# Optimization experiments

Measured on AMD Instinct MI355X. Metric: run time of the kernel, lower is better.

## Reference

```python
import jax, jax.numpy as jnp
import numpy as np

HEADS = 12
C = 384
FS = 56
WS = 7
WN = FS // WS            # windows per side = 8
NW = WN * WN             # total windows = 64
DISP = WS // 2           # cyclic shift displacement = 3
DK = (C / HEADS) ** (-0.5)


def _create_mask(ws, d, zero_dim=False, one_dim=False):
    m = np.zeros((ws * ws, ws * ws), np.float32)
    if zero_dim:
        m[-d * ws:, :-d * ws] = -np.inf
        m[:-d * ws, -d * ws:] = -np.inf
    if one_dim:
        t = np.zeros((ws, ws), np.float32)
        t[-d:, :-d] = -np.inf
        t[:-d, -d:] = -np.inf
        for i in range(0, ws * ws, ws):
            for j in range(0, ws * ws, ws):
                m[i:i + ws, j:j + ws] = t
    return m


def _window_mask():
    # per-window additive mask [NW, WS*WS, WS*WS] matching the torch slicing
    zm = _create_mask(WS, DISP, zero_dim=True)
    om = _create_mask(WS, DISP, one_dim=True)
    wm = np.zeros((NW, WS * WS, WS * WS), np.float32)
    wm[-WN:] += zm                 # last row of windows
    wm[WN - 1::WN] += om           # last column of windows
    return jnp.asarray(wm)


def _rel_indices():
    idx = np.array([[x, y] for x in range(WS) for y in range(WS)], np.int64)
    rel = idx[None, :, :] - idx[:, None, :] + WS - 1   # [WS^2, WS^2, 2]
    return rel


def _dconv(x, w):
    # depthwise 3x3, padding=1
    return jax.lax.conv_general_dilated(
        x, w, (1, 1), ((1, 1), (1, 1)),
        dimension_numbers=('NCHW', 'OIHW', 'NCHW'),
        feature_group_count=w.shape[0])


def _pconv(x, w, b):
    y = jax.lax.conv_general_dilated(
        x, w, (1, 1), 'VALID', dimension_numbers=('NCHW', 'OIHW', 'NCHW'))
    return y + b[None, :, None, None]


def _to_windows(t):
    # [B, C, H, W] -> [B, heads, NW, WS*WS, head_dim]
    B = t.shape[0]
    hd = C // HEADS
    t = t.reshape(B, HEADS, hd, WN, WS, WN, WS)
    t = t.transpose(0, 1, 3, 5, 4, 6, 2)
    return t.reshape(B, HEADS, NW, WS * WS, hd)


def _from_windows(t):
    # [B, heads, NW, WS*WS, head_dim] -> [B, C, H, W]
    B = t.shape[0]
    hd = C // HEADS
    t = t.reshape(B, HEADS, WN, WN, WS, WS, hd)
    t = t.transpose(0, 1, 6, 2, 4, 3, 5)
    return t.reshape(B, C, FS, FS)


def setup_inputs() -> dict:
    key = jax.random.key(0)
    ks = jax.random.split(key, 8)
    s = 0.05
    return {
        'x': jax.random.normal(ks[0], (16, C, FS, FS), jnp.float32),
        'qkv_dw': jax.random.normal(ks[1], (C, 1, 3, 3), jnp.float32) * s,
        'qkv_pw': jax.random.normal(ks[2], (3 * C, C, 1, 1), jnp.float32) * s,
        'qkv_pb': jax.random.normal(ks[3], (3 * C,), jnp.float32) * s,
        'out_dw': jax.random.normal(ks[4], (C, 1, 3, 3), jnp.float32) * s,
        'out_pw': jax.random.normal(ks[5], (C, C, 1, 1), jnp.float32) * s,
        'out_pb': jax.random.normal(ks[6], (C,), jnp.float32) * s,
        'pos_emb': jax.random.normal(ks[7], (2 * WS - 1, 2 * WS - 1), jnp.float32),
    }


def reference(x, qkv_dw, qkv_pw, qkv_pb, out_dw, out_pw, out_pb, pos_emb):
    rel = _rel_indices()
    wmask = _window_mask()

    x = jnp.roll(x, shift=(-DISP, -DISP), axis=(2, 3))       # cyclic shift
    x = _dconv(x, qkv_dw)
    qkv = _pconv(x, qkv_pw, qkv_pb)
    q, k, v = jnp.split(qkv, 3, axis=1)
    q, k, v = _to_windows(q), _to_windows(k), _to_windows(v)

    dots = jnp.einsum('bhwid,bhwjd->bhwij', q, k) * DK
    bias = pos_emb[rel[:, :, 0], rel[:, :, 1]]               # [WS^2, WS^2]
    dots = dots + bias[None, None, None] + wmask[None, None]

    attn = jax.nn.softmax(dots, axis=-1)
    out = jnp.einsum('bhwij,bhwjd->bhwid', attn, v)
    out = _from_windows(out)

    out = jnp.roll(out, shift=(DISP, DISP), axis=(2, 3))     # cyclic back shift
    out = _dconv(out, out_dw)
    out = _pconv(out, out_pw, out_pb)
    return out
```

## Files before the change

kernel.cpp:

```cpp
#include <hip/hip_runtime.h>
#include <hip/hip_bf16.h>
#include <cstddef>
#include <cstdint>

#define BQ    16
#define CC    384
#define C3    1152
#define HH    56
#define HWP   3136
#define NTOT  (BQ * HWP)
#define NHEAD 12
#define HD    32
#define WSZ   7
#define NWIN  64
#define WSQ   49
#define DKS   0.17677669529663687f

typedef __attribute__((ext_vector_type(8))) short bf16x8;
typedef __attribute__((ext_vector_type(4))) float f32x4;

union U128 { uint4 u; bf16x8 v; ushort us[8]; uint ui[4]; };

__device__ __forceinline__ ushort f2b(float f) {
    __hip_bfloat16 h = __float2bfloat16(f);
    return *reinterpret_cast<ushort*>(&h);
}
__device__ __forceinline__ float b2f(ushort u) {
    __hip_bfloat16 h;
    *reinterpret_cast<ushort*>(&h) = u;
    return __bfloat162float(h);
}

__global__ void cvt_bf16(const float* __restrict__ in, ushort* __restrict__ out, int n) {
    const int i = blockIdx.x * 256 + threadIdx.x;
    if (i < n) out[i] = f2b(in[i]);
}

__global__ void prep_mask(const float* __restrict__ pos, float* __restrict__ M) {
    const int idx = blockIdx.x * 256 + threadIdx.x;
    const int v = idx >> 12, rem = idx & 4095;
    const int j = rem >> 6, i = rem & 63;
    float m = -1e30f;
    if (i < WSQ && j < WSQ) {
        const int pir = i / WSZ, pic = i - pir * WSZ;
        const int pjr = j / WSZ, pjc = j - pjr * WSZ;
        const bool msk = ((v & 2) && ((pir >= 4) != (pjr >= 4))) ||
                         ((v & 1) && ((pic >= 4) != (pjc >= 4)));
        m = msk ? -1e30f : pos[(pjr - pir + 6) * 13 + (pjc - pic + 6)];
    }
    M[idx] = m;
}

template <bool BF16IN, int S>
__global__ __launch_bounds__(256) void dconv_px(const void* __restrict__ inv,
                                                const float* __restrict__ dw,
                                                ushort* __restrict__ out) {
    __shared__ ushort pl[6][32][68];
    const int band = blockIdx.x, cg = blockIdx.y, b = blockIdx.z;
    const int i0 = band * 4;
    const int t = threadIdx.x;
    const int ch = t & 31;

    float wreg[9];
    #pragma unroll
    for (int k = 0; k < 9; ++k) wreg[k] = dw[(cg * 32 + ch) * 9 + k];

    if (BF16IN) {
        const ushort* src = (const ushort*)inv;
        const int c8 = t & 3, sc = t >> 2;
        const int cc = sc < 56 ? sc : sc - 56;
        #pragma unroll
        for (int lr = 0; lr < 6; ++lr) {
            const int gi = i0 + lr - 1;
            U128 u; u.u = make_uint4(0, 0, 0, 0);
            if (gi >= 0 && gi < HH) {
                int rr = gi + S; if (rr >= HH) rr -= HH;
                u.u = *(const uint4*)&src[(size_t)(b * HWP + rr * HH + cc) * CC + cg * 32 + c8 * 8];
            }
            #pragma unroll
            for (int k2 = 0; k2 < 8; ++k2) pl[lr][c8 * 8 + k2][sc] = u.us[k2];
        }
    } else {
        const float* src = (const float*)inv;
        const int cq = t & 15, q0 = t >> 4;
        const int scb = cq < 14 ? cq * 4 : cq * 4 - 56;
        #pragma unroll
        for (int k = 0; k < 12; ++k) {
            const int pair = q0 + k * 16;
            const int lc = pair & 31, lr = pair >> 5;
            const int gi = i0 + lr - 1;
            float4 v = make_float4(0.f, 0.f, 0.f, 0.f);
            if (gi >= 0 && gi < HH) {
                int rr = gi + S; if (rr >= HH) rr -= HH;
                v = *(const float4*)&src[((size_t)(b * CC + cg * 32 + lc)) * HWP + rr * HH + scb];
            }
            ushort4 w;
            w.x = f2b(v.x); w.y = f2b(v.y); w.z = f2b(v.z); w.w = f2b(v.w);
            *(ushort4*)&pl[lr][lc][cq * 4] = w;
        }
    }
    __syncthreads();

    const int u = t >> 5;
    #pragma unroll
    for (int iter = 0; iter < 7; ++iter) {
        const int unit = iter * 8 + u;
        const int colb = unit >> 2;
        const int row  = unit & 3;
        const int c0 = colb * 4;
        int sc0 = c0 - 1 + S; if (sc0 >= HH) sc0 -= HH;
        float acc[4] = {0.f, 0.f, 0.f, 0.f};
        #pragma unroll
        for (int di = 0; di < 3; ++di) {
            const ushort* rp = &pl[row + di][ch][0];
            float v[6];
            #pragma unroll
            for (int k = 0; k < 6; ++k) v[k] = b2f(rp[sc0 + k]);
            if (colb == 0)  v[0] = 0.f;
            if (colb == 13) v[5] = 0.f;
            #pragma unroll
            for (int cc2 = 0; cc2 < 4; ++cc2) {
                acc[cc2] += wreg[di * 3 + 0] * v[cc2];
                acc[cc2] += wreg[di * 3 + 1] * v[cc2 + 1];
                acc[cc2] += wreg[di * 3 + 2] * v[cc2 + 2];
            }
        }
        const int orow = i0 + row;
        #pragma unroll
        for (int cc2 = 0; cc2 < 4; ++cc2)
            out[(size_t)(b * HWP + orow * HH + c0 + cc2) * CC + cg * 32 + ch] = f2b(acc[cc2]);
    }
}

template <int OC, bool OUT_BF16>
__global__ __launch_bounds__(256) void pconv_mfma(const ushort* __restrict__ bt,
                                                  const ushort* __restrict__ wa,
                                                  const float* __restrict__ bias,
                                                  void* __restrict__ outv) {
    __shared__ __align__(16) char smem[OUT_BF16 ? 34816 : 32768];

    const int nwg = gridDim.x;
    const int cpx = nwg >> 3;
    const int id  = blockIdx.x;
    const int wg  = (id & 7) * cpx + (id >> 3);
    const int oc0 = (wg % (OC / 128)) * 128;
    const int n0  = (wg / (OC / 128)) * 128;

    const int t   = threadIdx.x;
    const int l   = t & 63;
    const int wm  = (t >> 6) >> 1, wn = (t >> 6) & 1;
    const int i15 = l & 15, g = l >> 4;

    f32x4 acc[4][4] = {};

    const int r0 = t >> 2;
    const int kc = ((t & 3) ^ ((t >> 3) & 3)) * 8;
    const size_t gA0 = (size_t)(oc0 + r0) * CC + kc;
    const size_t gA1 = (size_t)(oc0 + r0 + 64) * CC + kc;
    const size_t gB0 = (size_t)(n0 + r0) * CC + kc;
    const size_t gB1 = (size_t)(n0 + r0 + 64) * CC + kc;
    const int ldsOff = (t & 192) * 16;

#define STAGE(buf, k0) do {                                                              \
    char* la_ = smem + (buf) * 16384 + ldsOff;                                           \
    char* lb_ = la_ + 8192;                                                              \
    __builtin_amdgcn_global_load_lds(                                                    \
        (const __attribute__((address_space(1))) void*)(wa + gA0 + (k0)),                \
        (__attribute__((address_space(3))) void*)la_, 16, 0, 0);                         \
    __builtin_amdgcn_global_load_lds(                                                    \
        (const __attribute__((address_space(1))) void*)(wa + gA1 + (k0)),                \
        (__attribute__((address_space(3))) void*)(la_ + 4096), 16, 0, 0);                \
    __builtin_amdgcn_global_load_lds(                                                    \
        (const __attribute__((address_space(1))) void*)(bt + gB0 + (k0)),                \
        (__attribute__((address_space(3))) void*)lb_, 16, 0, 0);                         \
    __builtin_amdgcn_global_load_lds(                                                    \
        (const __attribute__((address_space(1))) void*)(bt + gB1 + (k0)),                \
        (__attribute__((address_space(3))) void*)(lb_ + 4096), 16, 0, 0);                \
} while (0)

    const int colb = (g ^ ((i15 >> 1) & 3)) << 4;
    const int rbA = (wm * 64 + i15) * 64 + colb;
    const int rbB = (wn * 64 + i15) * 64 + colb;

    STAGE(0, 0);
    int cur = 0;
    for (int kt = 0; kt < 12; ++kt) {
        if (kt < 11) {
            STAGE(cur ^ 1, (kt + 1) * 32);
            asm volatile("s_waitcnt vmcnt(4)" ::: "memory");
        } else {
            asm volatile("s_waitcnt vmcnt(0)" ::: "memory");
        }
        __builtin_amdgcn_s_barrier();
        const char* bufA = smem + cur * 16384;
        const char* bufB = bufA + 8192;
        bf16x8 a[4], bb[4];
        #pragma unroll
        for (int i = 0; i < 4; ++i) {
            a[i]  = *(const bf16x8*)(bufA + rbA + i * 1024);
            bb[i] = *(const bf16x8*)(bufB + rbB + i * 1024);
        }
        #pragma unroll
        for (int mf = 0; mf < 4; ++mf)
            #pragma unroll
            for (int nf = 0; nf < 4; ++nf)
                acc[mf][nf] = __builtin_amdgcn_mfma_f32_16x16x32_bf16(a[mf], bb[nf], acc[mf][nf], 0, 0, 0);
        __builtin_amdgcn_sched_barrier(0);
        __builtin_amdgcn_s_barrier();
        cur ^= 1;
    }
#undef STAGE

    const int rl = (l >> 4) * 4;
    const int cl = l & 15;
    if (OUT_BF16) {
        ushort (* const sD)[136] = (ushort(*)[136])smem;
        #pragma unroll
        for (int mf = 0; mf < 4; ++mf) {
            const int ocl = wm * 64 + mf * 16 + rl;
            #pragma unroll
            for (int nf = 0; nf < 4; ++nf) {
                const int nl = wn * 64 + nf * 16 + cl;
                ushort4 w4;
                w4.x = f2b(acc[mf][nf][0] + bias[oc0 + ocl + 0]);
                w4.y = f2b(acc[mf][nf][1] + bias[oc0 + ocl + 1]);
                w4.z = f2b(acc[mf][nf][2] + bias[oc0 + ocl + 2]);
                w4.w = f2b(acc[mf][nf][3] + bias[oc0 + ocl + 3]);
                *(ushort4*)&sD[nl][ocl] = w4;
            }
        }
        __syncthreads();
        ushort* outp = (ushort*)outv;
        #pragma unroll
        for (int rr = 0; rr < 8; ++rr) {
            const int r = (t >> 4) + rr * 16;
            const int c8 = (t & 15) * 8;
            *(uint4*)&outp[(size_t)(n0 + r) * C3 + oc0 + c8] = *(const uint4*)&sD[r][c8];
        }
    } else {
        float* outp = (float*)outv;
        #pragma unroll
        for (int mf = 0; mf < 4; ++mf) {
            const int row = oc0 + wm * 64 + mf * 16 + rl;
            #pragma unroll
            for (int r = 0; r < 4; ++r) {
                const float bs = bias[row + r];
                #pragma unroll
                for (int nf = 0; nf < 4; ++nf) {
                    const int n = n0 + wn * 64 + nf * 16 + cl;
                    const int b = n / HWP, p = n - b * HWP;
                    outp[((size_t)b * OC + row + r) * HWP + p] = acc[mf][nf][r] + bs;
                }
            }
        }
    }
}

__global__ __launch_bounds__(256) void attn_mfma(const ushort* __restrict__ qkv,
                                                 const float* __restrict__ M,
                                                 ushort* __restrict__ out) {
    __shared__ __align__(16) ushort sV[4][64 * 40];

    const int w = blockIdx.x, hg = blockIdx.y, b = blockIdx.z;
    const int wr = w >> 3, wc = w & 7;
    const int t = threadIdx.x, ww = t >> 6, l = t & 63;
    const int h = hg * 4 + ww;
    const int i15 = l & 15, g = l >> 4;
    const int hch = h * HD;
    ushort* const sVw = sV[ww];
    const float* __restrict__ Mv = M + ((((wr == 7) ? 2 : 0) | ((wc == 7) ? 1 : 0)) << 12);

    #pragma unroll
    for (int pass = 0; pass < 4; ++pass) {
        const int e = l + pass * 64;
        const int pix = e >> 2, c8 = e & 3;
        uint4 v = make_uint4(0, 0, 0, 0);
        if (pix < WSQ) {
            const int n = b * HWP + (wr * WSZ + pix / 7) * HH + wc * WSZ + pix % 7;
            v = *(const uint4*)&qkv[(size_t)n * C3 + 2 * CC + hch + c8 * 8];
        }
        const int cst = c8 ^ ((pix >> 2) & 3);
        *(uint4*)&sVw[pix * 40 + cst * 8] = v;
    }

    bf16x8 qf[4], kf[4];
    #pragma unroll
    for (int it = 0; it < 4; ++it) {
        const int i = it * 16 + i15;
        U128 uq, uk;
        uq.u = make_uint4(0, 0, 0, 0);
        uk.u = make_uint4(0, 0, 0, 0);
        if (i < WSQ) {
            const int n = b * HWP + (wr * WSZ + i / 7) * HH + wc * WSZ + i % 7;
            uq.u = *(const uint4*)&qkv[(size_t)n * C3 + hch + g * 8];
            uk.u = *(const uint4*)&qkv[(size_t)n * C3 + CC + hch + g * 8];
        }
        qf[it] = uq.v;
        kf[it] = uk.v;
    }

    f32x4 sS[4][4] = {};
    #pragma unroll
    for (int jt = 0; jt < 4; ++jt)
        #pragma unroll
        for (int it = 0; it < 4; ++it)
            sS[jt][it] = __builtin_amdgcn_mfma_f32_16x16x32_bf16(kf[jt], qf[it], sS[jt][it], 0, 0, 0);

    #pragma unroll
    for (int jt = 0; jt < 4; ++jt) {
        #pragma unroll
        for (int r = 0; r < 4; ++r) {
            const float* mrow = Mv + (jt * 16 + 4 * g + r) * 64 + i15;
            #pragma unroll
            for (int it = 0; it < 4; ++it)
                sS[jt][it][r] = fmaf(sS[jt][it][r], DKS, mrow[it * 16]);
        }
    }

    #pragma unroll
    for (int it = 0; it < 4; ++it) {
        float m = -1e30f;
        #pragma unroll
        for (int jt = 0; jt < 4; ++jt)
            #pragma unroll
            for (int r = 0; r < 4; ++r) m = fmaxf(m, sS[jt][it][r]);
        m = fmaxf(m, __shfl_xor(m, 16));
        m = fmaxf(m, __shfl_xor(m, 32));
        float sum = 0.f;
        #pragma unroll
        for (int jt = 0; jt < 4; ++jt)
            #pragma unroll
            for (int r = 0; r < 4; ++r) {
                const float e2 = __expf(sS[jt][it][r] - m);
                sS[jt][it][r] = e2;
                sum += e2;
            }
        sum += __shfl_xor(sum, 16);
        sum += __shfl_xor(sum, 32);
        const float inv = 1.f / sum;
        #pragma unroll
        for (int jt = 0; jt < 4; ++jt)
            #pragma unroll
            for (int r = 0; r < 4; ++r) sS[jt][it][r] *= inv;
    }

    uint plo[4][4], phi[4][4];
    #pragma unroll
    for (int it = 0; it < 4; ++it)
        #pragma unroll
        for (int jt = 0; jt < 4; ++jt) {
            plo[it][jt] = (uint)f2b(sS[jt][it][0]) | ((uint)f2b(sS[jt][it][1]) << 16);
            phi[it][jt] = (uint)f2b(sS[jt][it][2]) | ((uint)f2b(sS[jt][it][3]) << 16);
        }

    const int srcLo = (2 * (g & 1)) * 16 + i15;
    const int srcHi = srcLo + 16;
    const bool oddHalf = ((g >> 1) & 1) != 0;

    f32x4 oacc[4][2] = {};
    #pragma unroll
    for (int kt = 0; kt < 2; ++kt) {
        bf16x8 bv[2];
        #pragma unroll
        for (int nt = 0; nt < 2; ++nt) {
            U128 u;
            #pragma unroll
            for (int s = 0; s < 8; ++s) {
                const int j = kt * 32 + 8 * g + s;
                const int d = nt * 16 + i15;
                const int cp = (d >> 3) ^ ((j >> 2) & 3);
                u.us[s] = sVw[j * 40 + cp * 8 + (d & 7)];
            }
            bv[nt] = u.v;
        }
        #pragma unroll
        for (int mt = 0; mt < 4; ++mt) {
            U128 pu;
            #pragma unroll
            for (int u2 = 0; u2 < 4; ++u2) {
                const int sl = (u2 >> 1) ? srcHi : srcLo;
                const uint vE = __shfl((u2 & 1) ? phi[mt][2 * kt]     : plo[mt][2 * kt],     sl, 64);
                const uint vO = __shfl((u2 & 1) ? phi[mt][2 * kt + 1] : plo[mt][2 * kt + 1], sl, 64);
                pu.ui[u2] = oddHalf ? vO : vE;
            }
            #pragma unroll
            for (int nt = 0; nt < 2; ++nt)
                oacc[mt][nt] = __builtin_amdgcn_mfma_f32_16x16x32_bf16(pu.v, bv[nt], oacc[mt][nt], 0, 0, 0);
        }
    }

    #pragma unroll
    for (int mt = 0; mt < 4; ++mt)
        #pragma unroll
        for (int nt = 0; nt < 2; ++nt)
            #pragma unroll
            for (int r = 0; r < 4; ++r) {
                const int i = mt * 16 + 4 * g + r;
                const int d = nt * 16 + i15;
                const int cp = (d >> 3) ^ ((i >> 2) & 3);
                sVw[i * 40 + cp * 8 + (d & 7)] = f2b(oacc[mt][nt][r]);
            }

    #pragma unroll
    for (int pass = 0; pass < 4; ++pass) {
        const int e = l + pass * 64;
        const int pix = e >> 2, c8 = e & 3;
        if (pix < WSQ) {
            const int n = b * HWP + (wr * WSZ + pix / 7) * HH + wc * WSZ + pix % 7;
            const int cp = c8 ^ ((pix >> 2) & 3);
            *(uint4*)&out[(size_t)n * CC + hch + c8 * 8] = *(const uint4*)&sVw[pix * 40 + cp * 8];
        }
    }
}

extern "C" void kernel_launch(void* const* d_in, const int* in_sizes, int n_in,
                              void* d_out, int out_size, void* d_ws, size_t ws_size,
                              hipStream_t stream) {
    const float* x      = (const float*)d_in[0];
    const float* qkv_dw = (const float*)d_in[1];
    const float* qkv_pw = (const float*)d_in[2];
    const float* qkv_pb = (const float*)d_in[3];
    const float* out_dw = (const float*)d_in[4];
    const float* out_pw = (const float*)d_in[5];
    const float* out_pb = (const float*)d_in[6];
    const float* pos    = (const float*)d_in[7];

    ushort* A   = (ushort*)d_ws;
    ushort* B   = A + (size_t)NTOT * CC;
    ushort* wA1 = B + (size_t)NTOT * C3;
    ushort* wA2 = wA1 + (size_t)C3 * CC;
    float*  Mw  = (float*)(wA2 + (size_t)CC * CC);

    cvt_bf16<<<(C3 * CC + 255) / 256, 256, 0, stream>>>(qkv_pw, wA1, C3 * CC);
    cvt_bf16<<<(CC * CC + 255) / 256, 256, 0, stream>>>(out_pw, wA2, CC * CC);
    prep_mask<<<64, 256, 0, stream>>>(pos, Mw);

    dconv_px<false, 3><<<dim3(14, 12, BQ), 256, 0, stream>>>(x, qkv_dw, A);
    pconv_mfma<C3, true><<<dim3((C3 / 128) * (NTOT / 128)), 256, 0, stream>>>(A, wA1, qkv_pb, B);
    attn_mfma<<<dim3(NWIN, NHEAD / 4, BQ), 256, 0, stream>>>(B, Mw, A);
    dconv_px<true, 53><<<dim3(14, 12, BQ), 256, 0, stream>>>(A, out_dw, B);
    pconv_mfma<CC, false><<<dim3((CC / 128) * (NTOT / 128)), 256, 0, stream>>>(B, wA2, out_pb, (float*)d_out);
}
```

Measured before the change: 198.2 us.

## Load weight fragments directly to registers and deepen B-tile LDS pipeline

The pointwise-conv GEMM now reads weight (A) fragments straight from global memory into double-buffered registers instead of staging them through LDS. Activation (B) tiles use a 4-slot LDS ring with a prefetch distance of two, and the second barrier per iteration is removed. The aim is to halve LDS staging traffic, cut barrier stalls and overlap more global latency with MFMA work. In exchange it adds uncoalesced per-lane global loads for A and more register pressure, and the final iterations issue wasted wrap-around prefetches.

```diff
diff --git a/kernel.cpp b/kernel.cpp
--- a/kernel.cpp
+++ b/kernel.cpp
@@ -155,21 +155,12 @@
 
     const int r0 = t >> 2;
     const int kc = ((t & 3) ^ ((t >> 3) & 3)) * 8;
-    const size_t gA0 = (size_t)(oc0 + r0) * CC + kc;
-    const size_t gA1 = (size_t)(oc0 + r0 + 64) * CC + kc;
     const size_t gB0 = (size_t)(n0 + r0) * CC + kc;
     const size_t gB1 = (size_t)(n0 + r0 + 64) * CC + kc;
     const int ldsOff = (t & 192) * 16;
 
-#define STAGE(buf, k0) do {                                                              \
-    char* la_ = smem + (buf) * 16384 + ldsOff;                                           \
-    char* lb_ = la_ + 8192;                                                              \
-    __builtin_amdgcn_global_load_lds(                                                    \
-        (const __attribute__((address_space(1))) void*)(wa + gA0 + (k0)),                \
-        (__attribute__((address_space(3))) void*)la_, 16, 0, 0);                         \
-    __builtin_amdgcn_global_load_lds(                                                    \
-        (const __attribute__((address_space(1))) void*)(wa + gA1 + (k0)),                \
-        (__attribute__((address_space(3))) void*)(la_ + 4096), 16, 0, 0);                \
+#define STAGE_B(buf, k0) do {                                                            \
+    char* lb_ = smem + (buf) * 8192 + ldsOff;                                            \
     __builtin_amdgcn_global_load_lds(                                                    \
         (const __attribute__((address_space(1))) void*)(bt + gB0 + (k0)),                \
         (__attribute__((address_space(3))) void*)lb_, 16, 0, 0);                         \
@@ -178,38 +169,44 @@
         (__attribute__((address_space(3))) void*)(lb_ + 4096), 16, 0, 0);                \
 } while (0)
 
+    const ushort* wrow = wa + (size_t)(oc0 + wm * 64 + i15) * CC + g * 8;
+
     const int colb = (g ^ ((i15 >> 1) & 3)) << 4;
-    const int rbA = (wm * 64 + i15) * 64 + colb;
     const int rbB = (wn * 64 + i15) * 64 + colb;
 
-    STAGE(0, 0);
-    int cur = 0;
+    bf16x8 af[2][4];
+
+    STAGE_B(0, 0);
+    STAGE_B(1, 32);
+    #pragma unroll
+    for (int i = 0; i < 4; ++i)
+        af[0][i] = *(const bf16x8*)(wrow + (size_t)i * 16 * CC);
+
+    #pragma unroll 2
     for (int kt = 0; kt < 12; ++kt) {
-        if (kt < 11) {
-            STAGE(cur ^ 1, (kt + 1) * 32);
-            asm volatile("s_waitcnt vmcnt(4)" ::: "memory");
-        } else {
-            asm volatile("s_waitcnt vmcnt(0)" ::: "memory");
-        }
+        const int kS = (kt + 2) % 12;
+        STAGE_B((kt + 2) & 3, kS * 32);
+        const int kA = (kt + 1) % 12;
+        #pragma unroll
+        for (int i = 0; i < 4; ++i)
+            af[(kt + 1) & 1][i] = *(const bf16x8*)(wrow + (size_t)i * 16 * CC + kA * 32);
+        asm volatile("s_waitcnt vmcnt(6)" ::: "memory");
         __builtin_amdgcn_s_barrier();
-        const char* bufA = smem + cur * 16384;
-        const char* bufB = bufA + 8192;
-        bf16x8 a[4], bb[4];
-        #pragma unroll
-        for (int i = 0; i < 4; ++i) {
-            a[i]  = *(const bf16x8*)(bufA + rbA + i * 1024);
+        const char* bufB = smem + (kt & 3) * 8192;
+        bf16x8 bb[4];
+        #pragma unroll
+        for (int i = 0; i < 4; ++i)
             bb[i] = *(const bf16x8*)(bufB + rbB + i * 1024);
-        }
         #pragma unroll
         for (int mf = 0; mf < 4; ++mf)
             #pragma unroll
             for (int nf = 0; nf < 4; ++nf)
-                acc[mf][nf] = __builtin_amdgcn_mfma_f32_16x16x32_bf16(a[mf], bb[nf], acc[mf][nf], 0, 0, 0);
-        __builtin_amdgcn_sched_barrier(0);
-        __builtin_amdgcn_s_barrier();
-        cur ^= 1;
-    }
-#undef STAGE
+                acc[mf][nf] = __builtin_amdgcn_mfma_f32_16x16x32_bf16(af[kt & 1][mf], bb[nf], acc[mf][nf], 0, 0, 0);
+    }
+#undef STAGE_B
+
+    asm volatile("s_waitcnt vmcnt(0)" ::: "memory");
+    __builtin_amdgcn_s_barrier();
 
     const int rl = (l >> 4) * 4;
     const int cl = l & 15;
```

Result: slower. 257.3 us (+29.9%).
